# Kernel optimization log

Hardware: AMD Instinct MI355X
Metric: run time of the kernel (lower is better)

Reference implementation:

```python
import jax, jax.numpy as jnp
import numpy as np

SIGMA_PRIOR = 0.5   # sigma init kwarg; logvar_prior = log(sigma), sigma_prior = exp(logvar_prior) = sigma
TEMP = 1.0
LN_EPS = 1e-5
DIM, NQ, NK = 256, 512, 512


def setup_inputs() -> dict:
    key = jax.random.key(0)
    ks = jax.random.split(key, 10)
    s = 1.0 / np.sqrt(DIM)
    return {
        "Q": jax.random.normal(ks[0], (NQ, DIM), jnp.float32),
        "K": jax.random.normal(ks[1], (NK, DIM), jnp.float32),
        "V": jax.random.normal(ks[2], (NK, DIM), jnp.float32),
        "eps": jax.random.normal(ks[3], (NQ, NK), jnp.float32),
        # prior MLP: Linear(dim,dim) -> ReLU -> Linear(dim,1)
        "W1p": jax.random.normal(ks[4], (DIM, DIM), jnp.float32) * s,
        "b1p": jnp.zeros((DIM,), jnp.float32),
        "w2p": jax.random.normal(ks[5], (DIM,), jnp.float32) * s,
        "b2p": jnp.zeros((), jnp.float32),
        # posterior MLP: Linear(2*dim, dim) -> ReLU
        "Wpost": jax.random.normal(ks[6], (DIM, 2 * DIM), jnp.float32) * s,
        "bpost": jnp.zeros((DIM,), jnp.float32),
        # mu / logvar heads: Linear(dim, 1)
        "w_mu": jax.random.normal(ks[7], (DIM,), jnp.float32) * s,
        "b_mu": jnp.zeros((), jnp.float32),
        "w_lv": jax.random.normal(ks[8], (DIM,), jnp.float32) * s,
        "b_lv": jnp.zeros((), jnp.float32),
        # output LayerNorm(dim)
        "gamma": jnp.ones((DIM,), jnp.float32),
        "beta": jnp.zeros((DIM,), jnp.float32),
    }


def reference(Q, K, V, eps, W1p, b1p, w2p, b2p, Wpost, bpost,
              w_mu, b_mu, w_lv, b_lv, gamma, beta):
    dim = Q.shape[-1]
    sigma_prior = jnp.float32(SIGMA_PRIOR)

    # --- prior: mlp_prior(K) per key; broadcast over queries (identical math to K_exp) ---
    h = jax.nn.relu(K @ W1p.T + b1p)                       # [Nk, dim]
    mu_prior = h @ w2p + b2p - 0.5 * sigma_prior ** 2      # [Nk]

    # --- posterior: Linear on cat([Q_exp, K_exp]) == Q@Wq^T + K@Wk^T + b ---
    Wq, Wk = Wpost[:, :dim], Wpost[:, dim:]
    latent = jax.nn.relu((Q @ Wq.T)[:, None, :] + (K @ Wk.T + bpost)[None, :, :])  # [Nq, Nk, dim]
    phi = latent @ w_mu + b_mu                             # [Nq, Nk]
    logvar = latent @ w_lv + b_lv                          # [Nq, Nk]
    sig = jnp.exp(0.5 * logvar)
    mu = phi - 0.5 * sig ** 2

    # --- KL(prior || posterior form used by the module) ---
    term0 = jnp.log(sigma_prior / sig)
    term1 = (sig ** 2 + (mu - mu_prior[None, :]) ** 2) / (2.0 * sigma_prior ** 2)
    kl = jnp.mean(term0 + term1 - 0.5)

    # --- reparameterized sample, softmax weights, context ---
    samples = jnp.exp(mu + sig * eps) / TEMP               # [Nq, Nk]
    weights = jax.nn.softmax(samples, axis=-1)
    context = weights @ V                                  # [Nq, dim]

    # --- LayerNorm(dim) ---
    m = jnp.mean(context, axis=-1, keepdims=True)
    v = jnp.var(context, axis=-1, keepdims=True)
    out = (context - m) / jnp.sqrt(v + LN_EPS) * gamma + beta
    return (out, kl)
```

## Files before the change

### kernel.cpp

```cpp
#include <hip/hip_runtime.h>
#include <math.h>

#define DIM 256
#define NQ  512
#define NK  512

#define WS_A   0
#define WS_B   (NQ*DIM)
#define WS_MP  (WS_B + NK*DIM)
#define WS_S   (WS_MP + 512)
#define WS_P   (WS_S + NQ*NK)

__global__ __launch_bounds__(256) void k1_precompute(
    const float* __restrict__ Q, const float* __restrict__ Km,
    const float* __restrict__ W1p, const float* __restrict__ b1p,
    const float* __restrict__ w2p, const float* __restrict__ b2p,
    const float* __restrict__ Wpost, const float* __restrict__ bpost,
    float* __restrict__ A, float* __restrict__ B, float* __restrict__ mu_prior)
{
    __shared__ float X_lds[8][DIM];
    __shared__ float red[8][260];
    const int tid = threadIdx.x;
    const int bid = blockIdx.x;

    int job, r0, wstride, wcol;
    const float* X;
    const float* W;
    if (bid < 64)       { job = 0; r0 = bid * 8;         X = Q;  W = Wpost; wstride = 2*DIM; wcol = 0;   }
    else if (bid < 128) { job = 1; r0 = (bid - 64) * 8;  X = Km; W = Wpost; wstride = 2*DIM; wcol = DIM; }
    else                { job = 2; r0 = (bid - 128) * 8; X = Km; W = W1p;   wstride = DIM;   wcol = 0;   }

    #pragma unroll
    for (int i = 0; i < 2; ++i) {
        int f4 = tid * 2 + i;
        int row = f4 >> 6, c4 = f4 & 63;
        *(float4*)&X_lds[row][c4 * 4] = *(const float4*)&X[(r0 + row) * DIM + c4 * 4];
    }
    __syncthreads();

    const float* wrow = W + tid * wstride + wcol;
    float acc[8] = {0.f, 0.f, 0.f, 0.f, 0.f, 0.f, 0.f, 0.f};
    #pragma unroll 4
    for (int d0 = 0; d0 < DIM; d0 += 4) {
        float4 w4 = *(const float4*)&wrow[d0];
        #pragma unroll
        for (int r = 0; r < 8; ++r) {
            float4 x4 = *(const float4*)&X_lds[r][d0];
            acc[r] = fmaf(x4.x, w4.x, acc[r]);
            acc[r] = fmaf(x4.y, w4.y, acc[r]);
            acc[r] = fmaf(x4.z, w4.z, acc[r]);
            acc[r] = fmaf(x4.w, w4.w, acc[r]);
        }
    }

    if (job == 0) {
        #pragma unroll
        for (int r = 0; r < 8; ++r) A[(r0 + r) * DIM + tid] = acc[r];
    } else if (job == 1) {
        float bp = bpost[tid];
        #pragma unroll
        for (int r = 0; r < 8; ++r) B[(r0 + r) * DIM + tid] = acc[r] + bp;
    } else {
        float b1 = b1p[tid], w2 = w2p[tid];
        #pragma unroll
        for (int r = 0; r < 8; ++r) red[r][tid] = fmaxf(acc[r] + b1, 0.f) * w2;
        __syncthreads();
        int wid = tid >> 6, lane = tid & 63;
        float b2 = b2p[0];
        #pragma unroll
        for (int rr = 0; rr < 2; ++rr) {
            int r = wid * 2 + rr;
            float v = red[r][lane] + red[r][lane + 64] + red[r][lane + 128] + red[r][lane + 192];
            #pragma unroll
            for (int off = 32; off; off >>= 1) v += __shfl_xor(v, off);
            if (lane == 0) mu_prior[r0 + r] = v + b2 - 0.125f;
        }
    }
}

__global__ __launch_bounds__(256) void k2_latent(
    const float* __restrict__ A, const float* __restrict__ B,
    const float* __restrict__ mu_prior, const float* __restrict__ eps,
    const float* __restrict__ w_mu, const float* __restrict__ b_mu,
    const float* __restrict__ w_lv, const float* __restrict__ b_lv,
    float* __restrict__ samples, float* __restrict__ partials)
{
    __shared__ float A_lds[32][260];
    __shared__ float B_lds[32][260];
    __shared__ float wm[DIM], wl[DIM];
    __shared__ float wred[4];
    const int tid = threadIdx.x;
    const int bq0 = (blockIdx.x >> 4) * 32;
    const int bk0 = (blockIdx.x & 15) * 32;

    #pragma unroll
    for (int i = 0; i < 8; ++i) {
        int f4 = tid + 256 * i;
        int row = f4 >> 6, c4 = f4 & 63;
        *(float4*)&A_lds[row][c4 * 4] = *(const float4*)&A[(bq0 + row) * DIM + c4 * 4];
        *(float4*)&B_lds[row][c4 * 4] = *(const float4*)&B[(bk0 + row) * DIM + c4 * 4];
    }
    wm[tid] = w_mu[tid];
    wl[tid] = w_lv[tid];
    __syncthreads();

    const int tq = tid >> 4, tk = tid & 15;
    float p00 = 0, p01 = 0, p10 = 0, p11 = 0;
    float l00 = 0, l01 = 0, l10 = 0, l11 = 0;

    #pragma unroll 2
    for (int d0 = 0; d0 < DIM; d0 += 4) {
        float4 a0 = *(const float4*)&A_lds[tq][d0];
        float4 a1 = *(const float4*)&A_lds[tq + 16][d0];
        float4 b0 = *(const float4*)&B_lds[tk][d0];
        float4 b1 = *(const float4*)&B_lds[tk + 16][d0];
        float4 m4 = *(const float4*)&wm[d0];
        float4 v4 = *(const float4*)&wl[d0];
#define STEP(c) { float r_;                                                      \
        r_ = fmaxf(a0.c + b0.c, 0.f); p00 = fmaf(r_, m4.c, p00); l00 = fmaf(r_, v4.c, l00); \
        r_ = fmaxf(a0.c + b1.c, 0.f); p01 = fmaf(r_, m4.c, p01); l01 = fmaf(r_, v4.c, l01); \
        r_ = fmaxf(a1.c + b0.c, 0.f); p10 = fmaf(r_, m4.c, p10); l10 = fmaf(r_, v4.c, l10); \
        r_ = fmaxf(a1.c + b1.c, 0.f); p11 = fmaf(r_, m4.c, p11); l11 = fmaf(r_, v4.c, l11); }
        STEP(x) STEP(y) STEP(z) STEP(w)
#undef STEP
    }

    const float bmu = b_mu[0], blv = b_lv[0];
    const int qa = bq0 + tq, qb = qa + 16;
    const int ka = bk0 + tk, kb = ka + 16;
    const float mpa = mu_prior[ka], mpb = mu_prior[kb];
    const float C0 = -0.69314718056f - 0.5f;
    float kls = 0.f;

#define FINISH(pacc, lacc, q, k, mp) {                       \
        float lv   = (lacc) + blv;                           \
        float phi  = (pacc) + bmu;                           \
        float sig2 = expf(lv);                               \
        float sig  = expf(0.5f * lv);                        \
        float mu   = phi - 0.5f * sig2;                      \
        float dm   = mu - (mp);                              \
        kls += C0 - 0.5f * lv + 2.f * (sig2 + dm * dm);      \
        samples[(q) * NK + (k)] = expf(mu + sig * eps[(q) * NK + (k)]); }

    FINISH(p00, l00, qa, ka, mpa)
    FINISH(p01, l01, qa, kb, mpb)
    FINISH(p10, l10, qb, ka, mpa)
    FINISH(p11, l11, qb, kb, mpb)
#undef FINISH

    #pragma unroll
    for (int off = 32; off; off >>= 1) kls += __shfl_xor(kls, off);
    if ((tid & 63) == 0) wred[tid >> 6] = kls;
    __syncthreads();
    if (tid == 0) partials[blockIdx.x] = wred[0] + wred[1] + wred[2] + wred[3];
}

__global__ __launch_bounds__(256) void k3_output(
    const float* __restrict__ samples, const float* __restrict__ V,
    const float* __restrict__ gamma, const float* __restrict__ beta,
    const float* __restrict__ partials, float* __restrict__ out)
{
    __shared__ float w_lds[2][NK];
    __shared__ float redbuf[8][DIM];
    __shared__ float sred[4], sred2[4], klr[4];
    const int tid = threadIdx.x;
    const int q0 = blockIdx.x * 2;

    if (blockIdx.x == 0) {
        float v = partials[tid];
        #pragma unroll
        for (int off = 32; off; off >>= 1) v += __shfl_xor(v, off);
        if ((tid & 63) == 0) klr[tid >> 6] = v;
        __syncthreads();
        if (tid == 0) out[NQ * DIM] = (klr[0] + klr[1] + klr[2] + klr[3]) * (1.f / (float)(NQ * NK));
    }

    float inv[2];
    #pragma unroll
    for (int r = 0; r < 2; ++r) {
        float s0 = samples[(q0 + r) * NK + tid];
        float s1 = samples[(q0 + r) * NK + tid + 256];
        float m = fmaxf(s0, s1);
        #pragma unroll
        for (int off = 32; off; off >>= 1) m = fmaxf(m, __shfl_xor(m, off));
        if ((tid & 63) == 0) sred[tid >> 6] = m;
        __syncthreads();
        m = fmaxf(fmaxf(sred[0], sred[1]), fmaxf(sred[2], sred[3]));
        float e0 = expf(s0 - m), e1 = expf(s1 - m);
        w_lds[r][tid] = e0;
        w_lds[r][tid + 256] = e1;
        float sum = e0 + e1;
        #pragma unroll
        for (int off = 32; off; off >>= 1) sum += __shfl_xor(sum, off);
        __syncthreads();
        if ((tid & 63) == 0) sred[tid >> 6] = sum;
        __syncthreads();
        sum = sred[0] + sred[1] + sred[2] + sred[3];
        inv[r] = 1.f / sum;
        __syncthreads();
    }

    const int g = tid & 63, s = tid >> 6;
    float a00 = 0, a01 = 0, a02 = 0, a03 = 0;
    float a10 = 0, a11 = 0, a12 = 0, a13 = 0;
    const float* vp = V + s * 128 * DIM + 4 * g;
    #pragma unroll 4
    for (int i = 0; i < 128; ++i) {
        float4 v4 = *(const float4*)(vp + i * DIM);
        int k = s * 128 + i;
        float w0 = w_lds[0][k], w1 = w_lds[1][k];
        a00 = fmaf(w0, v4.x, a00); a01 = fmaf(w0, v4.y, a01);
        a02 = fmaf(w0, v4.z, a02); a03 = fmaf(w0, v4.w, a03);
        a10 = fmaf(w1, v4.x, a10); a11 = fmaf(w1, v4.y, a11);
        a12 = fmaf(w1, v4.z, a12); a13 = fmaf(w1, v4.w, a13);
    }
    *(float4*)&redbuf[s * 2 + 0][4 * g] = make_float4(a00, a01, a02, a03);
    *(float4*)&redbuf[s * 2 + 1][4 * g] = make_float4(a10, a11, a12, a13);
    __syncthreads();

    const float gm = gamma[tid], bt = beta[tid];
    #pragma unroll
    for (int r = 0; r < 2; ++r) {
        float c = redbuf[0 + r][tid] + redbuf[2 + r][tid] + redbuf[4 + r][tid] + redbuf[6 + r][tid];
        c *= inv[r];
        float s1v = c, s2v = c * c;
        #pragma unroll
        for (int off = 32; off; off >>= 1) {
            s1v += __shfl_xor(s1v, off);
            s2v += __shfl_xor(s2v, off);
        }
        if ((tid & 63) == 0) { sred[tid >> 6] = s1v; sred2[tid >> 6] = s2v; }
        __syncthreads();
        float mean = (sred[0] + sred[1] + sred[2] + sred[3]) * (1.f / DIM);
        float msq  = (sred2[0] + sred2[1] + sred2[2] + sred2[3]) * (1.f / DIM);
        float var  = msq - mean * mean;
        float o = (c - mean) / sqrtf(var + 1e-5f) * gm + bt;
        out[(q0 + r) * DIM + tid] = o;
        __syncthreads();
    }
}

extern "C" void kernel_launch(void* const* d_in, const int* in_sizes, int n_in,
                              void* d_out, int out_size, void* d_ws, size_t ws_size,
                              hipStream_t stream)
{
    (void)in_sizes; (void)n_in; (void)out_size; (void)ws_size;
    const float* Q     = (const float*)d_in[0];
    const float* K     = (const float*)d_in[1];
    const float* V     = (const float*)d_in[2];
    const float* eps   = (const float*)d_in[3];
    const float* W1p   = (const float*)d_in[4];
    const float* b1p   = (const float*)d_in[5];
    const float* w2p   = (const float*)d_in[6];
    const float* b2p   = (const float*)d_in[7];
    const float* Wpost = (const float*)d_in[8];
    const float* bpost = (const float*)d_in[9];
    const float* w_mu  = (const float*)d_in[10];
    const float* b_mu  = (const float*)d_in[11];
    const float* w_lv  = (const float*)d_in[12];
    const float* b_lv  = (const float*)d_in[13];
    const float* gamma = (const float*)d_in[14];
    const float* beta  = (const float*)d_in[15];
    float* out = (float*)d_out;
    float* wsf = (float*)d_ws;

    float* A        = wsf + WS_A;
    float* B        = wsf + WS_B;
    float* mu_prior = wsf + WS_MP;
    float* samples  = wsf + WS_S;
    float* partials = wsf + WS_P;

    k1_precompute<<<dim3(192), dim3(256), 0, stream>>>(
        Q, K, W1p, b1p, w2p, b2p, Wpost, bpost, A, B, mu_prior);
    k2_latent<<<dim3(256), dim3(256), 0, stream>>>(
        A, B, mu_prior, eps, w_mu, b_mu, w_lv, b_lv, samples, partials);
    k3_output<<<dim3(256), dim3(256), 0, stream>>>(
        samples, V, gamma, beta, partials, out);
}
```

Baseline: 128.9 us.

## Split reduction dimension across 512-thread blocks in all three kernels

```diff
diff --git a/kernel.cpp b/kernel.cpp
--- a/kernel.cpp
+++ b/kernel.cpp
@@ -11,74 +11,86 @@
 #define WS_S   (WS_MP + 512)
 #define WS_P   (WS_S + NQ*NK)
 
-__global__ __launch_bounds__(256) void k1_precompute(
+__global__ __launch_bounds__(512) void k1_precompute(
     const float* __restrict__ Q, const float* __restrict__ Km,
     const float* __restrict__ W1p, const float* __restrict__ b1p,
     const float* __restrict__ w2p, const float* __restrict__ b2p,
     const float* __restrict__ Wpost, const float* __restrict__ bpost,
     float* __restrict__ A, float* __restrict__ B, float* __restrict__ mu_prior)
 {
-    __shared__ float X_lds[8][DIM];
-    __shared__ float red[8][260];
+    __shared__ float X_lds[4][DIM];
+    __shared__ float red[2][4][260];
     const int tid = threadIdx.x;
     const int bid = blockIdx.x;
 
-    int job, r0, wstride, wcol;
-    const float* X;
-    const float* W;
-    if (bid < 64)       { job = 0; r0 = bid * 8;         X = Q;  W = Wpost; wstride = 2*DIM; wcol = 0;   }
-    else if (bid < 128) { job = 1; r0 = (bid - 64) * 8;  X = Km; W = Wpost; wstride = 2*DIM; wcol = DIM; }
-    else                { job = 2; r0 = (bid - 128) * 8; X = Km; W = W1p;   wstride = DIM;   wcol = 0;   }
-
-    #pragma unroll
-    for (int i = 0; i < 2; ++i) {
-        int f4 = tid * 2 + i;
-        int row = f4 >> 6, c4 = f4 & 63;
+    const int job = bid >> 7;
+    const int r0  = (bid & 127) * 4;
+    const float* X = (job == 0) ? Q : Km;
+    const float* W = (job == 2) ? W1p : Wpost;
+    const int wstride = (job == 2) ? DIM : 2 * DIM;
+    const int wcol    = (job == 1) ? DIM : 0;
+
+    if (tid < 256) {
+        int row = tid >> 6, c4 = tid & 63;
         *(float4*)&X_lds[row][c4 * 4] = *(const float4*)&X[(r0 + row) * DIM + c4 * 4];
     }
     __syncthreads();
 
-    const float* wrow = W + tid * wstride + wcol;
-    float acc[8] = {0.f, 0.f, 0.f, 0.f, 0.f, 0.f, 0.f, 0.f};
-    #pragma unroll 4
-    for (int d0 = 0; d0 < DIM; d0 += 4) {
+    const int c  = tid & 255;
+    const int dh = tid >> 8;
+    const float* wrow = W + c * wstride + wcol + dh * 128;
+    const float* xrow0 = &X_lds[0][dh * 128];
+
+    float acc0 = 0.f, acc1 = 0.f, acc2 = 0.f, acc3 = 0.f;
+    #pragma unroll 8
+    for (int d0 = 0; d0 < 128; d0 += 4) {
         float4 w4 = *(const float4*)&wrow[d0];
-        #pragma unroll
-        for (int r = 0; r < 8; ++r) {
-            float4 x4 = *(const float4*)&X_lds[r][d0];
-            acc[r] = fmaf(x4.x, w4.x, acc[r]);
-            acc[r] = fmaf(x4.y, w4.y, acc[r]);
-            acc[r] = fmaf(x4.z, w4.z, acc[r]);
-            acc[r] = fmaf(x4.w, w4.w, acc[r]);
-        }
-    }
-
-    if (job == 0) {
-        #pragma unroll
-        for (int r = 0; r < 8; ++r) A[(r0 + r) * DIM + tid] = acc[r];
-    } else if (job == 1) {
-        float bp = bpost[tid];
-        #pragma unroll
-        for (int r = 0; r < 8; ++r) B[(r0 + r) * DIM + tid] = acc[r] + bp;
+        float4 x0 = *(const float4*)&xrow0[d0];
+        float4 x1 = *(const float4*)&xrow0[DIM + d0];
+        float4 x2 = *(const float4*)&xrow0[2 * DIM + d0];
+        float4 x3 = *(const float4*)&xrow0[3 * DIM + d0];
+        acc0 = fmaf(x0.x, w4.x, acc0); acc0 = fmaf(x0.y, w4.y, acc0);
+        acc0 = fmaf(x0.z, w4.z, acc0); acc0 = fmaf(x0.w, w4.w, acc0);
+        acc1 = fmaf(x1.x, w4.x, acc1); acc1 = fmaf(x1.y, w4.y, acc1);
+        acc1 = fmaf(x1.z, w4.z, acc1); acc1 = fmaf(x1.w, w4.w, acc1);
+        acc2 = fmaf(x2.x, w4.x, acc2); acc2 = fmaf(x2.y, w4.y, acc2);
+        acc2 = fmaf(x2.z, w4.z, acc2); acc2 = fmaf(x2.w, w4.w, acc2);
+        acc3 = fmaf(x3.x, w4.x, acc3); acc3 = fmaf(x3.y, w4.y, acc3);
+        acc3 = fmaf(x3.z, w4.z, acc3); acc3 = fmaf(x3.w, w4.w, acc3);
+    }
+    red[dh][0][c] = acc0; red[dh][1][c] = acc1;
+    red[dh][2][c] = acc2; red[dh][3][c] = acc3;
+    __syncthreads();
+
+    if (job < 2) {
+        if (tid < 256) {
+            #pragma unroll
+            for (int r = 0; r < 4; ++r) {
+                float v = red[0][r][c] + red[1][r][c];
+                if (job == 0) A[(r0 + r) * DIM + c] = v;
+                else          B[(r0 + r) * DIM + c] = v + bpost[c];
+            }
+        }
     } else {
-        float b1 = b1p[tid], w2 = w2p[tid];
-        #pragma unroll
-        for (int r = 0; r < 8; ++r) red[r][tid] = fmaxf(acc[r] + b1, 0.f) * w2;
-        __syncthreads();
-        int wid = tid >> 6, lane = tid & 63;
-        float b2 = b2p[0];
-        #pragma unroll
-        for (int rr = 0; rr < 2; ++rr) {
-            int r = wid * 2 + rr;
-            float v = red[r][lane] + red[r][lane + 64] + red[r][lane + 128] + red[r][lane + 192];
+        if (tid < 256) {
+            float b1 = b1p[c], w2 = w2p[c];
+            #pragma unroll
+            for (int r = 0; r < 4; ++r)
+                red[0][r][c] = fmaxf(red[0][r][c] + red[1][r][c] + b1, 0.f) * w2;
+        }
+        __syncthreads();
+        int w = tid >> 6, lane = tid & 63;
+        if (w < 4) {
+            float v = red[0][w][lane] + red[0][w][lane + 64]
+                    + red[0][w][lane + 128] + red[0][w][lane + 192];
             #pragma unroll
             for (int off = 32; off; off >>= 1) v += __shfl_xor(v, off);
-            if (lane == 0) mu_prior[r0 + r] = v + b2 - 0.125f;
+            if (lane == 0) mu_prior[r0 + w] = v + b2p[0] - 0.125f;
         }
     }
 }
 
-__global__ __launch_bounds__(256) void k2_latent(
+__global__ __launch_bounds__(512) void k2_latent(
     const float* __restrict__ A, const float* __restrict__ B,
     const float* __restrict__ mu_prior, const float* __restrict__ eps,
     const float* __restrict__ w_mu, const float* __restrict__ b_mu,
@@ -88,28 +100,33 @@
     __shared__ float A_lds[32][260];
     __shared__ float B_lds[32][260];
     __shared__ float wm[DIM], wl[DIM];
-    __shared__ float wred[4];
+    __shared__ float red[2][256][9];
+    __shared__ float wred[8];
     const int tid = threadIdx.x;
     const int bq0 = (blockIdx.x >> 4) * 32;
     const int bk0 = (blockIdx.x & 15) * 32;
 
     #pragma unroll
-    for (int i = 0; i < 8; ++i) {
-        int f4 = tid + 256 * i;
+    for (int i = 0; i < 4; ++i) {
+        int f4 = tid + 512 * i;
         int row = f4 >> 6, c4 = f4 & 63;
         *(float4*)&A_lds[row][c4 * 4] = *(const float4*)&A[(bq0 + row) * DIM + c4 * 4];
         *(float4*)&B_lds[row][c4 * 4] = *(const float4*)&B[(bk0 + row) * DIM + c4 * 4];
     }
-    wm[tid] = w_mu[tid];
-    wl[tid] = w_lv[tid];
-    __syncthreads();
-
-    const int tq = tid >> 4, tk = tid & 15;
+    if (tid < 256) { wm[tid] = w_mu[tid]; wl[tid] = w_lv[tid]; }
+    __syncthreads();
+
+    const int l  = tid & 255;
+    const int dh = tid >> 8;
+    const int tq = l >> 4, tk = l & 15;
+    const int db = dh * 128;
+
     float p00 = 0, p01 = 0, p10 = 0, p11 = 0;
     float l00 = 0, l01 = 0, l10 = 0, l11 = 0;
 
-    #pragma unroll 2
-    for (int d0 = 0; d0 < DIM; d0 += 4) {
+    #pragma unroll 4
+    for (int dd = 0; dd < 128; dd += 4) {
+        int d0 = db + dd;
         float4 a0 = *(const float4*)&A_lds[tq][d0];
         float4 a1 = *(const float4*)&A_lds[tq + 16][d0];
         float4 b0 = *(const float4*)&B_lds[tk][d0];
@@ -125,89 +142,111 @@
 #undef STEP
     }
 
-    const float bmu = b_mu[0], blv = b_lv[0];
-    const int qa = bq0 + tq, qb = qa + 16;
-    const int ka = bk0 + tk, kb = ka + 16;
-    const float mpa = mu_prior[ka], mpb = mu_prior[kb];
-    const float C0 = -0.69314718056f - 0.5f;
+    red[dh][l][0] = p00; red[dh][l][1] = l00;
+    red[dh][l][2] = p01; red[dh][l][3] = l01;
+    red[dh][l][4] = p10; red[dh][l][5] = l10;
+    red[dh][l][6] = p11; red[dh][l][7] = l11;
+    __syncthreads();
+
     float kls = 0.f;
-
-#define FINISH(pacc, lacc, q, k, mp) {                       \
-        float lv   = (lacc) + blv;                           \
-        float phi  = (pacc) + bmu;                           \
-        float sig2 = expf(lv);                               \
-        float sig  = expf(0.5f * lv);                        \
-        float mu   = phi - 0.5f * sig2;                      \
-        float dm   = mu - (mp);                              \
-        kls += C0 - 0.5f * lv + 2.f * (sig2 + dm * dm);      \
-        samples[(q) * NK + (k)] = expf(mu + sig * eps[(q) * NK + (k)]); }
-
-    FINISH(p00, l00, qa, ka, mpa)
-    FINISH(p01, l01, qa, kb, mpb)
-    FINISH(p10, l10, qb, ka, mpa)
-    FINISH(p11, l11, qb, kb, mpb)
+    if (tid < 256) {
+        const float bmu = b_mu[0], blv = b_lv[0];
+        const int qa = bq0 + tq, qb = qa + 16;
+        const int ka = bk0 + tk, kb = ka + 16;
+        const float mpa = mu_prior[ka], mpb = mu_prior[kb];
+        const float C0 = -0.69314718056f - 0.5f;
+
+#define FINISH(i, q, k, mp) {                                        \
+        float pacc = red[0][tid][2*(i)]   + red[1][tid][2*(i)];      \
+        float lacc = red[0][tid][2*(i)+1] + red[1][tid][2*(i)+1];    \
+        float lv   = lacc + blv;                                     \
+        float phi  = pacc + bmu;                                     \
+        float sig  = __expf(0.5f * lv);                              \
+        float sig2 = sig * sig;                                      \
+        float mu   = phi - 0.5f * sig2;                              \
+        float dm   = mu - (mp);                                      \
+        kls += C0 - 0.5f * lv + 2.f * (sig2 + dm * dm);              \
+        samples[(q) * NK + (k)] = __expf(mu + sig * eps[(q) * NK + (k)]); }
+
+        FINISH(0, qa, ka, mpa)
+        FINISH(1, qa, kb, mpb)
+        FINISH(2, qb, ka, mpa)
+        FINISH(3, qb, kb, mpb)
 #undef FINISH
+    }
 
     #pragma unroll
     for (int off = 32; off; off >>= 1) kls += __shfl_xor(kls, off);
     if ((tid & 63) == 0) wred[tid >> 6] = kls;
     __syncthreads();
-    if (tid == 0) partials[blockIdx.x] = wred[0] + wred[1] + wred[2] + wred[3];
+    if (tid == 0) {
+        float s = 0.f;
+        #pragma unroll
+        for (int i = 0; i < 8; ++i) s += wred[i];
+        partials[blockIdx.x] = s;
+    }
 }
 
-__global__ __launch_bounds__(256) void k3_output(
+__global__ __launch_bounds__(512) void k3_output(
     const float* __restrict__ samples, const float* __restrict__ V,
     const float* __restrict__ gamma, const float* __restrict__ beta,
     const float* __restrict__ partials, float* __restrict__ out)
 {
     __shared__ float w_lds[2][NK];
-    __shared__ float redbuf[8][DIM];
-    __shared__ float sred[4], sred2[4], klr[4];
+    __shared__ float redbuf[16][DIM];
+    __shared__ float sred[8], sred2[8], klr[8], sinv[2];
     const int tid = threadIdx.x;
     const int q0 = blockIdx.x * 2;
 
     if (blockIdx.x == 0) {
-        float v = partials[tid];
+        float v = (tid < 256) ? partials[tid] : 0.f;
         #pragma unroll
         for (int off = 32; off; off >>= 1) v += __shfl_xor(v, off);
         if ((tid & 63) == 0) klr[tid >> 6] = v;
         __syncthreads();
-        if (tid == 0) out[NQ * DIM] = (klr[0] + klr[1] + klr[2] + klr[3]) * (1.f / (float)(NQ * NK));
-    }
-
-    float inv[2];
+        if (tid == 0) {
+            float s = 0.f;
+            #pragma unroll
+            for (int i = 0; i < 8; ++i) s += klr[i];
+            out[NQ * DIM] = s * (1.f / (float)(NQ * NK));
+        }
+    }
+
     #pragma unroll
     for (int r = 0; r < 2; ++r) {
-        float s0 = samples[(q0 + r) * NK + tid];
-        float s1 = samples[(q0 + r) * NK + tid + 256];
-        float m = fmaxf(s0, s1);
+        float sv = samples[(q0 + r) * NK + tid];
+        float m = sv;
         #pragma unroll
         for (int off = 32; off; off >>= 1) m = fmaxf(m, __shfl_xor(m, off));
         if ((tid & 63) == 0) sred[tid >> 6] = m;
         __syncthreads();
-        m = fmaxf(fmaxf(sred[0], sred[1]), fmaxf(sred[2], sred[3]));
-        float e0 = expf(s0 - m), e1 = expf(s1 - m);
-        w_lds[r][tid] = e0;
-        w_lds[r][tid + 256] = e1;
-        float sum = e0 + e1;
+        m = fmaxf(fmaxf(fmaxf(sred[0], sred[1]), fmaxf(sred[2], sred[3])),
+                  fmaxf(fmaxf(sred[4], sred[5]), fmaxf(sred[6], sred[7])));
+        float e = __expf(sv - m);
+        w_lds[r][tid] = e;
+        float sum = e;
         #pragma unroll
         for (int off = 32; off; off >>= 1) sum += __shfl_xor(sum, off);
         __syncthreads();
         if ((tid & 63) == 0) sred[tid >> 6] = sum;
         __syncthreads();
-        sum = sred[0] + sred[1] + sred[2] + sred[3];
-        inv[r] = 1.f / sum;
+        if (tid == 0) {
+            float s = 0.f;
+            #pragma unroll
+            for (int i = 0; i < 8; ++i) s += sred[i];
+            sinv[r] = 1.f / s;
+        }
         __syncthreads();
     }
 
     const int g = tid & 63, s = tid >> 6;
     float a00 = 0, a01 = 0, a02 = 0, a03 = 0;
     float a10 = 0, a11 = 0, a12 = 0, a13 = 0;
-    const float* vp = V + s * 128 * DIM + 4 * g;
-    #pragma unroll 4
-    for (int i = 0; i < 128; ++i) {
+    const float* vp = V + s * 64 * DIM + 4 * g;
+    #pragma unroll 8
+    for (int i = 0; i < 64; ++i) {
         float4 v4 = *(const float4*)(vp + i * DIM);
-        int k = s * 128 + i;
+        int k = s * 64 + i;
         float w0 = w_lds[0][k], w1 = w_lds[1][k];
         a00 = fmaf(w0, v4.x, a00); a01 = fmaf(w0, v4.y, a01);
         a02 = fmaf(w0, v4.z, a02); a03 = fmaf(w0, v4.w, a03);
@@ -218,26 +257,23 @@
     *(float4*)&redbuf[s * 2 + 1][4 * g] = make_float4(a10, a11, a12, a13);
     __syncthreads();
 
-    const float gm = gamma[tid], bt = beta[tid];
-    #pragma unroll
-    for (int r = 0; r < 2; ++r) {
-        float c = redbuf[0 + r][tid] + redbuf[2 + r][tid] + redbuf[4 + r][tid] + redbuf[6 + r][tid];
-        c *= inv[r];
-        float s1v = c, s2v = c * c;
-        #pragma unroll
-        for (int off = 32; off; off >>= 1) {
-            s1v += __shfl_xor(s1v, off);
-            s2v += __shfl_xor(s2v, off);
-        }
-        if ((tid & 63) == 0) { sred[tid >> 6] = s1v; sred2[tid >> 6] = s2v; }
-        __syncthreads();
-        float mean = (sred[0] + sred[1] + sred[2] + sred[3]) * (1.f / DIM);
-        float msq  = (sred2[0] + sred2[1] + sred2[2] + sred2[3]) * (1.f / DIM);
-        float var  = msq - mean * mean;
-        float o = (c - mean) / sqrtf(var + 1e-5f) * gm + bt;
-        out[(q0 + r) * DIM + tid] = o;
-        __syncthreads();
-    }
+    const int r = tid >> 8, col = tid & 255;
+    float c = 0.f;
+    #pragma unroll
+    for (int j = 0; j < 8; ++j) c += redbuf[j * 2 + r][col];
+    c *= sinv[r];
+    float s1v = c, s2v = c * c;
+    #pragma unroll
+    for (int off = 32; off; off >>= 1) {
+        s1v += __shfl_xor(s1v, off);
+        s2v += __shfl_xor(s2v, off);
+    }
+    if ((tid & 63) == 0) { sred[tid >> 6] = s1v; sred2[tid >> 6] = s2v; }
+    __syncthreads();
+    float mean = (sred[4 * r] + sred[4 * r + 1] + sred[4 * r + 2] + sred[4 * r + 3]) * (1.f / DIM);
+    float msq  = (sred2[4 * r] + sred2[4 * r + 1] + sred2[4 * r + 2] + sred2[4 * r + 3]) * (1.f / DIM);
+    float var  = msq - mean * mean;
+    out[(q0 + r) * DIM + col] = (c - mean) * rsqrtf(var + 1e-5f) * gamma[col] + beta[col];
 }
 
 extern "C" void kernel_launch(void* const* d_in, const int* in_sizes, int n_in,
@@ -270,10 +306,10 @@
     float* samples  = wsf + WS_S;
     float* partials = wsf + WS_P;
 
-    k1_precompute<<<dim3(192), dim3(256), 0, stream>>>(
+    k1_precompute<<<dim3(384), dim3(512), 0, stream>>>(
         Q, K, W1p, b1p, w2p, b2p, Wpost, bpost, A, B, mu_prior);
-    k2_latent<<<dim3(256), dim3(256), 0, stream>>>(
+    k2_latent<<<dim3(256), dim3(512), 0, stream>>>(
         A, B, mu_prior, eps, w_mu, b_mu, w_lv, b_lv, samples, partials);
-    k3_output<<<dim3(256), dim3(256), 0, stream>>>(
+    k3_output<<<dim3(256), dim3(512), 0, stream>>>(
         samples, V, gamma, beta, partials, out);
 }
```

Result: faster. 123.2 us (-4.4%).
